# Kernel tuning notes

Measured on AMD Instinct MI355X. Metric: run time of the kernel, lower is better.

## Reference

```python
import math
import jax, jax.numpy as jnp
import numpy as np

FILTER_ORDER = 64
FILTER_EMB_DIM = 5
HIDDEN = 256
SHIFT = 0.05
FAST_DECAY_PCT = 0.3
SLOW_DECAY_PCT = 1.5
TARGET = 0.01


def setup_inputs() -> dict:
    key = jax.random.key(0)
    ks = jax.random.split(key, 8)
    B, C, L = 8, HIDDEN, 8192

    def lin_w(k, fan_out, fan_in):
        return jax.random.normal(k, (fan_out, fan_in), jnp.float32) / np.sqrt(fan_in).astype(np.float32)

    return {
        "x": jax.random.normal(ks[0], (B, C, L), jnp.float32),
        "W1": lin_w(ks[1], FILTER_ORDER, FILTER_EMB_DIM),
        "b1": jnp.zeros((FILTER_ORDER,), jnp.float32),
        "freq0": jnp.ones((1, FILTER_ORDER), jnp.float32),
        "W2": lin_w(ks[2], FILTER_ORDER, FILTER_ORDER),
        "b2": jnp.zeros((FILTER_ORDER,), jnp.float32),
        "freq1": jnp.ones((1, FILTER_ORDER), jnp.float32),
        "W3": lin_w(ks[3], FILTER_ORDER, FILTER_ORDER),
        "b3": jnp.zeros((FILTER_ORDER,), jnp.float32),
        "freq2": jnp.ones((1, FILTER_ORDER), jnp.float32),
        "Wout": lin_w(ks[4], HIDDEN, FILTER_ORDER),
        "D": jax.random.normal(ks[5], (HIDDEN,), jnp.float32),
        "L": L,
    }


def _pos_emb(L):
    # HyenaDnaPositionalEmbedding: z (1, L, emb_dim), t (1, L, 1)
    t = jnp.linspace(0.0, 1.0, L, dtype=jnp.float32)[None, :, None]
    t_rescaled = jnp.linspace(0.0, L - 1, L, dtype=jnp.float32)[None, :, None]
    w = 2.0 * math.pi * t_rescaled / L  # (1, L, 1)
    bands = (FILTER_EMB_DIM - 1) // 2
    f = jnp.linspace(1e-4, bands - 1, bands, dtype=jnp.float32)[None, None]  # (1, 1, bands)
    z = jnp.concatenate([t, jnp.cos(-f * w), jnp.sin(-f * w)], axis=-1)  # (1, L, emb_dim)
    return z, t


def _filter_kernel(W1, b1, freq0, W2, b2, freq1, W3, b3, freq2, Wout, L):
    z, t = _pos_emb(L)
    h = jnp.sin(freq0 * (jnp.einsum('ble,oe->blo', z, W1) + b1))
    h = jnp.sin(freq1 * (jnp.einsum('blo,po->blp', h, W2) + b2))
    h = jnp.sin(freq2 * (jnp.einsum('blo,po->blp', h, W3) + b3))
    h = jnp.einsum('blo,do->bld', h, Wout)  # (1, L, HIDDEN)
    # exponential modulation window
    max_decay = math.log(TARGET) / FAST_DECAY_PCT
    min_decay = math.log(TARGET) / SLOW_DECAY_PCT
    deltas = jnp.linspace(min_decay, max_decay, HIDDEN, dtype=jnp.float32)[None, None]
    decay = jnp.exp(-t * jnp.abs(deltas))  # (1, L, HIDDEN)
    h = h * (decay + SHIFT)
    return h[0].T  # (HIDDEN, L) channels-major kernel


def _fftconv(u, k, D):
    # y = conv(u, k) + u * D via FFT, zero-padded to 2L (linear convolution)
    L = u.shape[-1]
    fft_size = 2 * L
    k_f = jnp.fft.rfft(k.astype(jnp.float32), n=fft_size) / fft_size  # (C, fft_size//2+1)
    u_f = jnp.fft.rfft(u.astype(jnp.float32), n=fft_size)             # (B, C, fft_size//2+1)
    y = jnp.fft.irfft(u_f * k_f, n=fft_size, norm='forward')[..., :L]
    return (y + u * D[:, None]).astype(u.dtype)


def reference(x, W1, b1, freq0, W2, b2, freq1, W3, b3, freq2, Wout, D, L):
    k = _filter_kernel(W1, b1, freq0, W2, b2, freq1, W3, b3, freq2, Wout, L)
    return _fftconv(x, k, D)
```

## Files before the change

### kernel.cpp

```cpp
#include <hip/hip_runtime.h>

#define L_SEQ 8192
#define NTH 512
#define HID 256
#define PIDX(i) ((i) + ((i) >> 4))
#define LDS_SZ 8704

#define ANG16 3.83495196971410315e-4f
#define ANG8  7.66990393942820630e-4f
#define CS16 0.99999992646571789f
#define SN16 3.83495187571395563e-4f
#define CS8  0.99999970586287223f
#define SN8  7.66990318742704490e-4f
#define C707 0.70710678118654752f

__device__ __forceinline__ float2 cmul(float2 a, float2 b) {
  return make_float2(a.x*b.x - a.y*b.y, a.x*b.y + a.y*b.x);
}
__device__ __forceinline__ float2 cadd(float2 a, float2 b){ return make_float2(a.x+b.x, a.y+b.y); }
__device__ __forceinline__ float2 csub(float2 a, float2 b){ return make_float2(a.x-b.x, a.y-b.y); }

__device__ __forceinline__ void bf4_fwd(float2 a0, float2 a1, float2 a2, float2 a3,
                                        float2& o0, float2& o1, float2& o2, float2& o3) {
  float2 t0 = cadd(a0,a2), t1 = csub(a0,a2), t2 = cadd(a1,a3), t3 = csub(a1,a3);
  o0 = cadd(t0,t2);
  o2 = csub(t0,t2);
  o1 = make_float2(t1.x + t3.y, t1.y - t3.x);
  o3 = make_float2(t1.x - t3.y, t1.y + t3.x);
}
__device__ __forceinline__ void bf4_inv(float2 c0, float2 c1, float2 c2, float2 c3,
                                        float2& o0, float2& o1, float2& o2, float2& o3) {
  float2 u0 = cadd(c0,c2), u2 = csub(c0,c2), u1 = cadd(c1,c3);
  float2 v3 = make_float2(c3.y - c1.y, c1.x - c3.x);
  o0 = cadd(u0,u1); o2 = csub(u0,u1); o1 = cadd(u2,v3); o3 = csub(u2,v3);
}

__device__ __forceinline__ void fwd8(float2 P[8]) {
  float2 e0=cadd(P[0],P[4]), e1=cadd(P[1],P[5]), e2=cadd(P[2],P[6]), e3=cadd(P[3],P[7]);
  float2 o0=csub(P[0],P[4]), o1=csub(P[1],P[5]), o2=csub(P[2],P[6]), o3=csub(P[3],P[7]);
  o1 = make_float2((o1.x+o1.y)*C707, (o1.y-o1.x)*C707);
  o2 = make_float2(o2.y, -o2.x);
  o3 = make_float2((o3.y-o3.x)*C707, -(o3.x+o3.y)*C707);
  float2 q0,q1,q2,q3;
  bf4_fwd(e0,e1,e2,e3,q0,q1,q2,q3);
  P[0]=q0; P[2]=q1; P[4]=q2; P[6]=q3;
  bf4_fwd(o0,o1,o2,o3,q0,q1,q2,q3);
  P[1]=q0; P[3]=q1; P[5]=q2; P[7]=q3;
}
__device__ __forceinline__ void inv8(float2 P[8]) {
  float2 E0,E1,E2,E3,O0,O1,O2,O3;
  bf4_inv(P[0],P[2],P[4],P[6],E0,E1,E2,E3);
  bf4_inv(P[1],P[3],P[5],P[7],O0,O1,O2,O3);
  O1 = make_float2((O1.x-O1.y)*C707, (O1.x+O1.y)*C707);
  O2 = make_float2(-O2.y, O2.x);
  O3 = make_float2(-(O3.x+O3.y)*C707, (O3.x-O3.y)*C707);
  P[0]=cadd(E0,O0); P[4]=csub(E0,O0);
  P[1]=cadd(E1,O1); P[5]=csub(E1,O1);
  P[2]=cadd(E2,O2); P[6]=csub(E2,O2);
  P[3]=cadd(E3,O3); P[7]=csub(E3,O3);
}

template<int M>
__device__ __forceinline__ void fwd_stage8(float2* __restrict__ X, int t) {
  #pragma unroll
  for (int r = 0; r < 2; ++r) {
    int s = t + NTH*r;
    int i2 = s & (M-1);
    int g  = s / M;
    int base = g*8*M + i2;
    float2 P[8];
    #pragma unroll
    for (int j=0;j<8;++j) P[j] = X[PIDX(base + j*M)];
    fwd8(P);
    float sb, cb;
    __sincosf(-6.2831853071795864769f * (float)i2 / (float)(8*M), &sb, &cb);
    float2 w1 = make_float2(cb, sb);
    float2 w2 = cmul(w1,w1), w3 = cmul(w2,w1), w4 = cmul(w2,w2);
    float2 w5 = cmul(w4,w1), w6 = cmul(w4,w2), w7 = cmul(w4,w3);
    X[PIDX(base)]     = P[0];
    X[PIDX(base+M)]   = cmul(P[1],w1);
    X[PIDX(base+2*M)] = cmul(P[2],w2);
    X[PIDX(base+3*M)] = cmul(P[3],w3);
    X[PIDX(base+4*M)] = cmul(P[4],w4);
    X[PIDX(base+5*M)] = cmul(P[5],w5);
    X[PIDX(base+6*M)] = cmul(P[6],w6);
    X[PIDX(base+7*M)] = cmul(P[7],w7);
  }
}
template<int M>
__device__ __forceinline__ void inv_stage8(float2* __restrict__ X, int t) {
  #pragma unroll
  for (int r = 0; r < 2; ++r) {
    int s = t + NTH*r;
    int i2 = s & (M-1);
    int g  = s / M;
    int base = g*8*M + i2;
    float sb, cb;
    __sincosf(6.2831853071795864769f * (float)i2 / (float)(8*M), &sb, &cb);
    float2 w1 = make_float2(cb, sb);
    float2 w2 = cmul(w1,w1), w3 = cmul(w2,w1), w4 = cmul(w2,w2);
    float2 w5 = cmul(w4,w1), w6 = cmul(w4,w2), w7 = cmul(w4,w3);
    float2 P[8];
    P[0] = X[PIDX(base)];
    P[1] = cmul(X[PIDX(base+M)],  w1);
    P[2] = cmul(X[PIDX(base+2*M)],w2);
    P[3] = cmul(X[PIDX(base+3*M)],w3);
    P[4] = cmul(X[PIDX(base+4*M)],w4);
    P[5] = cmul(X[PIDX(base+5*M)],w5);
    P[6] = cmul(X[PIDX(base+6*M)],w6);
    P[7] = cmul(X[PIDX(base+7*M)],w7);
    inv8(P);
    #pragma unroll
    for (int j=0;j<8;++j) X[PIDX(base + j*M)] = P[j];
  }
}

__device__ __forceinline__ void fft_mid_fwd(float2* __restrict__ X, int t) {
  __syncthreads();
  fwd_stage8<512>(X,t); __syncthreads();
  fwd_stage8<64>(X,t);  __syncthreads();
  fwd_stage8<8>(X,t);   __syncthreads();
}
__device__ __forceinline__ void fft_mid_inv(float2* __restrict__ X, int t) {
  __syncthreads();
  inv_stage8<8>(X,t);   __syncthreads();
  inv_stage8<64>(X,t);  __syncthreads();
  inv_stage8<512>(X,t); __syncthreads();
}

__device__ __forceinline__ void middle_pointwise(float2* __restrict__ X,
                                                 const float2* __restrict__ K, int t) {
  #pragma unroll
  for (int r = 0; r < 2; ++r) {
    int base = 8*(t + NTH*r);
    float2 kreg[8];
    #pragma unroll
    for (int q=0;q<8;++q) kreg[q] = K[base+q];
    float2 P[8];
    #pragma unroll
    for (int q=0;q<8;++q) P[q] = X[PIDX(base+q)];
    fwd8(P);
    #pragma unroll
    for (int q=0;q<8;++q) P[q] = cmul(P[q], kreg[q]);
    inv8(P);
    #pragma unroll
    for (int q=0;q<8;++q) X[PIDX(base+q)] = P[q];
  }
}

__global__ __launch_bounds__(256) void mlp_kernel(
    const float* __restrict__ W1, const float* __restrict__ b1, const float* __restrict__ fq0,
    const float* __restrict__ W2, const float* __restrict__ b2, const float* __restrict__ fq1,
    const float* __restrict__ W3, const float* __restrict__ b3, const float* __restrict__ fq2,
    float* __restrict__ h3g) {
  __shared__ float hs[2][16][64];
  int tid = threadIdx.x;
  int lane = tid & 63, w = tid >> 6;
  int l0 = blockIdx.x * 16;

  float w1r[5];
  #pragma unroll
  for (int e = 0; e < 5; ++e) w1r[e] = W1[lane*5+e];
  float b1v = b1[lane], f0 = fq0[lane];
  #pragma unroll
  for (int r = 0; r < 4; ++r) {
    int l = l0 + w + 4*r;
    float t = (float)l * (1.0f / (float)(L_SEQ - 1));
    float ang = 6.2831853071795864769f * (float)l / (float)L_SEQ;
    float s0, c0, s1, c1;
    __sincosf(1e-4f * ang, &s0, &c0);
    __sincosf(ang, &s1, &c1);
    float acc = b1v + t*w1r[0] + c0*w1r[1] + c1*w1r[2] - s0*w1r[3] - s1*w1r[4];
    hs[0][w + 4*r][lane] = __sinf(f0 * acc);
  }
  __syncthreads();

  float wr[64];
  #pragma unroll
  for (int j = 0; j < 16; ++j) *(float4*)&wr[4*j] = *(const float4*)&W2[lane*64 + 4*j];
  float b2v = b2[lane], f1 = fq1[lane];
  #pragma unroll
  for (int r = 0; r < 4; ++r) {
    int ll = w + 4*r;
    float a0 = 0.f, a1 = 0.f, a2 = 0.f, a3 = 0.f;
    #pragma unroll
    for (int o = 0; o < 64; o += 4) {
      a0 += hs[0][ll][o+0] * wr[o+0];
      a1 += hs[0][ll][o+1] * wr[o+1];
      a2 += hs[0][ll][o+2] * wr[o+2];
      a3 += hs[0][ll][o+3] * wr[o+3];
    }
    hs[1][ll][lane] = __sinf(f1 * (b2v + ((a0+a1)+(a2+a3))));
  }
  __syncthreads();

  #pragma unroll
  for (int j = 0; j < 16; ++j) *(float4*)&wr[4*j] = *(const float4*)&W3[lane*64 + 4*j];
  float b3v = b3[lane], f2 = fq2[lane];
  #pragma unroll
  for (int r = 0; r < 4; ++r) {
    int ll = w + 4*r;
    float a0 = 0.f, a1 = 0.f, a2 = 0.f, a3 = 0.f;
    #pragma unroll
    for (int o = 0; o < 64; o += 4) {
      a0 += hs[1][ll][o+0] * wr[o+0];
      a1 += hs[1][ll][o+1] * wr[o+1];
      a2 += hs[1][ll][o+2] * wr[o+2];
      a3 += hs[1][ll][o+3] * wr[o+3];
    }
    h3g[(size_t)(l0 + ll) * 64 + lane] = __sinf(f2 * (b3v + ((a0+a1)+(a2+a3))));
  }
}

__global__ __launch_bounds__(256) void kwrite_kernel(const float* __restrict__ h3g,
                                                     const float* __restrict__ Wout,
                                                     const float* __restrict__ Dv,
                                                     float* __restrict__ kbuf) {
  __shared__ float tileh[256][65];
  int tid = threadIdx.x;
  int l0 = blockIdx.x * 256;
  int c0 = blockIdx.y * 32;
  {
    const float4* src = (const float4*)(h3g + (size_t)l0 * 64);
    #pragma unroll
    for (int q = 0; q < 16; ++q) {
      int idx = tid + 256*q;
      int row = idx >> 4, col4 = idx & 15;
      float4 v = src[idx];
      tileh[row][col4*4+0] = v.x;
      tileh[row][col4*4+1] = v.y;
      tileh[row][col4*4+2] = v.z;
      tileh[row][col4*4+3] = v.w;
    }
  }
  __syncthreads();
  float hr[64];
  #pragma unroll
  for (int o = 0; o < 64; ++o) hr[o] = tileh[tid][o];
  int l = l0 + tid;
  float t = (float)l * (1.0f / (float)(L_SEQ - 1));
  const float mind = -3.0701134573253945f;
  const float maxd = -15.350567286626972f;
  for (int jj = 0; jj < 32; ++jj) {
    int c = c0 + jj;
    float a0 = 0.f, a1 = 0.f, a2 = 0.f, a3 = 0.f;
    #pragma unroll
    for (int o = 0; o < 64; o += 4) {
      a0 += hr[o+0] * Wout[c*64+o+0];
      a1 += hr[o+1] * Wout[c*64+o+1];
      a2 += hr[o+2] * Wout[c*64+o+2];
      a3 += hr[o+3] * Wout[c*64+o+3];
    }
    float acc = (a0+a1)+(a2+a3);
    float delta = mind + (maxd - mind) * ((float)c * (1.0f/255.0f));
    float dec = __expf(-t * fabsf(delta)) + 0.05f;
    float v = acc * dec;
    if (l == 0) v += Dv[c];
    kbuf[(size_t)c * L_SEQ + l] = v;
  }
}

__global__ __launch_bounds__(NTH) void kf_kernel(const float* __restrict__ kbuf,
                                                 float2* __restrict__ Kf) {
  __shared__ float2 X[LDS_SZ];
  int pipe = blockIdx.x;
  int c = blockIdx.y;
  int t = threadIdx.x;
  const float* kr = kbuf + (size_t)c * L_SEQ;
  const float sc = 1.0f / 16384.0f;
  #pragma unroll
  for (int r = 0; r < 2; ++r) {
    int n0 = 4*t + 2048*r;
    float4 lo4 = *(const float4*)(kr + n0);
    float4 hi4 = *(const float4*)(kr + n0 + 4096);
    if (pipe == 0) {
      float sb, cb; __sincosf(-ANG8 * (float)n0, &sb, &cb);
      float2 w8 = make_float2(cb, sb);
      #pragma unroll
      for (int j = 0; j < 4; ++j) {
        if (j) w8 = cmul(w8, make_float2(CS8, -SN8));
        float klo = ((const float*)&lo4)[j];
        float khi = ((const float*)&hi4)[j];
        X[PIDX(n0+j)]      = make_float2(klo + khi, 0.f);
        float d = klo - khi;
        X[PIDX(n0+j+4096)] = make_float2(d * w8.x, d * w8.y);
      }
    } else {
      float sb, cb; __sincosf(-ANG16 * (float)n0, &sb, &cb);
      float2 w16 = make_float2(cb, sb);
      #pragma unroll
      for (int j = 0; j < 4; ++j) {
        if (j) w16 = cmul(w16, make_float2(CS16, -SN16));
        float klo = ((const float*)&lo4)[j];
        float khi = ((const float*)&hi4)[j];
        float2 vlo = make_float2(klo * w16.x, klo * w16.y);
        float2 vhi = make_float2(khi * w16.y, -khi * w16.x);
        float2 w8 = cmul(w16, w16);
        X[PIDX(n0+j)]      = cadd(vlo, vhi);
        X[PIDX(n0+j+4096)] = cmul(csub(vlo, vhi), w8);
      }
    }
  }
  fft_mid_fwd(X, t);
  #pragma unroll
  for (int r = 0; r < 2; ++r) {
    int base = 8*(t + NTH*r);
    float2 P[8];
    #pragma unroll
    for (int q=0;q<8;++q) P[q] = X[PIDX(base+q)];
    fwd8(P);
    float2* out = Kf + (size_t)c * 16384 + pipe*8192 + base;
    #pragma unroll
    for (int q=0;q<8;++q) out[q] = make_float2(P[q].x*sc, P[q].y*sc);
  }
}

__global__ __launch_bounds__(NTH) void conv_kernel(const float* __restrict__ x,
                                                   const float2* __restrict__ Kf,
                                                   float* __restrict__ y) {
  __shared__ float2 X[LDS_SZ];
  int c = blockIdx.x;
  int p = blockIdx.y;
  int t = threadIdx.x;
  const float* u0 = x + ((size_t)p       * HID + c) * L_SEQ;
  const float* u1 = x + ((size_t)(p + 4) * HID + c) * L_SEQ;
  const float2* KA = Kf + (size_t)c * 16384;
  const float2* KB = KA + 8192;
  float* y0 = y + ((size_t)p       * HID + c) * L_SEQ;
  float* y1 = y + ((size_t)(p + 4) * HID + c) * L_SEQ;

  #pragma unroll
  for (int r = 0; r < 2; ++r) {
    int n0 = 4*t + 2048*r;
    float4 a0 = *(const float4*)(u0 + n0);
    float4 a1 = *(const float4*)(u1 + n0);
    float4 b0 = *(const float4*)(u0 + n0 + 4096);
    float4 b1 = *(const float4*)(u1 + n0 + 4096);
    float sb, cb; __sincosf(-ANG16 * (float)n0, &sb, &cb);
    float2 w16 = make_float2(cb, sb);
    #pragma unroll
    for (int j = 0; j < 4; ++j) {
      if (j) w16 = cmul(w16, make_float2(CS16, -SN16));
      float2 vlo = cmul(make_float2(((const float*)&a0)[j], ((const float*)&a1)[j]), w16);
      float2 vhi = cmul(make_float2(((const float*)&b0)[j], ((const float*)&b1)[j]),
                        make_float2(w16.y, -w16.x));
      float2 w8 = cmul(w16, w16);
      X[PIDX(n0+j)]      = cadd(vlo, vhi);
      X[PIDX(n0+j+4096)] = cmul(csub(vlo, vhi), w8);
    }
  }
  fft_mid_fwd(X, t);
  middle_pointwise(X, KB, t);
  fft_mid_inv(X, t);
  float2 stash[16];
  #pragma unroll
  for (int r = 0; r < 2; ++r) {
    int n0 = 4*t + 2048*r;
    float sb, cb; __sincosf(ANG16 * (float)n0, &sb, &cb);
    float2 w16b = make_float2(cb, sb);
    #pragma unroll
    for (int j = 0; j < 4; ++j) {
      if (j) w16b = cmul(w16b, make_float2(CS16, SN16));
      float2 P = X[PIDX(n0+j)], Q = X[PIDX(n0+j+4096)];
      float2 w8b = cmul(w16b, w16b);
      float2 tt = cmul(Q, w8b);
      stash[r*4+j]     = cmul(cadd(P, tt), w16b);
      stash[8 + r*4+j] = cmul(csub(P, tt), make_float2(-w16b.y, w16b.x));
    }
  }
  __syncthreads();

  #pragma unroll
  for (int r = 0; r < 2; ++r) {
    int n0 = 4*t + 2048*r;
    float4 a0 = *(const float4*)(u0 + n0);
    float4 a1 = *(const float4*)(u1 + n0);
    float4 b0 = *(const float4*)(u0 + n0 + 4096);
    float4 b1 = *(const float4*)(u1 + n0 + 4096);
    float sb, cb; __sincosf(-ANG8 * (float)n0, &sb, &cb);
    float2 w8 = make_float2(cb, sb);
    #pragma unroll
    for (int j = 0; j < 4; ++j) {
      if (j) w8 = cmul(w8, make_float2(CS8, -SN8));
      float2 vlo = make_float2(((const float*)&a0)[j], ((const float*)&a1)[j]);
      float2 vhi = make_float2(((const float*)&b0)[j], ((const float*)&b1)[j]);
      X[PIDX(n0+j)]      = cadd(vlo, vhi);
      X[PIDX(n0+j+4096)] = cmul(csub(vlo, vhi), w8);
    }
  }
  fft_mid_fwd(X, t);
  middle_pointwise(X, KA, t);
  fft_mid_inv(X, t);
  #pragma unroll
  for (int r = 0; r < 2; ++r) {
    int n0 = 4*t + 2048*r;
    float sb, cb; __sincosf(ANG8 * (float)n0, &sb, &cb);
    float2 w8b = make_float2(cb, sb);
    float4 w00, w01, w10, w11;
    #pragma unroll
    for (int j = 0; j < 4; ++j) {
      if (j) w8b = cmul(w8b, make_float2(CS8, SN8));
      float2 P = X[PIDX(n0+j)], Q = X[PIDX(n0+j+4096)];
      float2 tt = cmul(Q, w8b);
      float2 lo = cadd(cadd(P, tt), stash[r*4+j]);
      float2 hi = cadd(csub(P, tt), stash[8 + r*4+j]);
      ((float*)&w00)[j] = lo.x; ((float*)&w01)[j] = lo.y;
      ((float*)&w10)[j] = hi.x; ((float*)&w11)[j] = hi.y;
    }
    *(float4*)(y0 + n0)        = w00;
    *(float4*)(y1 + n0)        = w01;
    *(float4*)(y0 + n0 + 4096) = w10;
    *(float4*)(y1 + n0 + 4096) = w11;
  }
}

extern "C" void kernel_launch(void* const* d_in, const int* in_sizes, int n_in,
                              void* d_out, int out_size, void* d_ws, size_t ws_size,
                              hipStream_t stream) {
  const float* x    = (const float*)d_in[0];
  const float* W1   = (const float*)d_in[1];
  const float* b1   = (const float*)d_in[2];
  const float* fq0  = (const float*)d_in[3];
  const float* W2   = (const float*)d_in[4];
  const float* b2   = (const float*)d_in[5];
  const float* fq1  = (const float*)d_in[6];
  const float* W3   = (const float*)d_in[7];
  const float* b3   = (const float*)d_in[8];
  const float* fq2  = (const float*)d_in[9];
  const float* Wout = (const float*)d_in[10];
  const float* Dv   = (const float*)d_in[11];

  float*  kbuf = (float*)d_ws;
  float2* Kf   = (float2*)((char*)d_ws + (size_t)HID * L_SEQ * sizeof(float));
  float*  h3g  = (float*)((char*)d_ws + 38ull*1024*1024);
  float*  y    = (float*)d_out;

  mlp_kernel   <<<dim3(512),   256, 0, stream>>>(W1,b1,fq0,W2,b2,fq1,W3,b3,fq2,h3g);
  kwrite_kernel<<<dim3(32, 8), 256, 0, stream>>>(h3g, Wout, Dv, kbuf);
  kf_kernel    <<<dim3(2, 256), NTH, 0, stream>>>(kbuf, Kf);
  conv_kernel  <<<dim3(256, 4), NTH, 0, stream>>>(x, Kf, y);
}
```

Before: 165.7 us.

## Vectorize radix-8 FFT stages with paired float4 LDS access and spill partial output to global

Changes LDS padding to two floats every 32 elements so adjacent complex pairs stay 16-byte aligned. The M=512 and M=64 stages now process two adjacent butterflies per thread using float4 LDS loads and stores, with the second twiddle derived by a constant rotation. The 16-element register stash that held the first half's result is removed: partial outputs are written to global y and re-read and accumulated after the second pass. This cuts register pressure and LDS instruction count, at the cost of extra global memory traffic.

```diff
diff --git a/kernel.cpp b/kernel.cpp
--- a/kernel.cpp
+++ b/kernel.cpp
@@ -3,7 +3,7 @@
 #define L_SEQ 8192
 #define NTH 512
 #define HID 256
-#define PIDX(i) ((i) + ((i) >> 4))
+#define PIDX(i) ((i) + (((i) >> 5) << 1))
 #define LDS_SZ 8704
 
 #define ANG16 3.83495196971410315e-4f
@@ -58,6 +58,71 @@
   P[1]=cadd(E1,O1); P[5]=csub(E1,O1);
   P[2]=cadd(E2,O2); P[6]=csub(E2,O2);
   P[3]=cadd(E3,O3); P[7]=csub(E3,O3);
+}
+
+template<int M> struct WS;
+template<> struct WS<512> { static constexpr float c = 0.99999882345170188f, s = 1.53398018628476561e-3f; };
+template<> struct WS<64>  { static constexpr float c = 0.99992470183914454f, s = 1.22715382857199261e-2f; };
+
+template<int M>
+__device__ __forceinline__ void fwd_stage8p(float2* __restrict__ X, int t) {
+  const int HM = M/2;
+  int g = t / HM;
+  int v = t - g*HM;
+  int i2 = 2*v;
+  int base = g*8*M + i2;
+  float2 P[8], Q[8];
+  #pragma unroll
+  for (int j=0;j<8;++j) {
+    float4 w = *(const float4*)&X[PIDX(base + j*M)];
+    P[j] = make_float2(w.x, w.y);
+    Q[j] = make_float2(w.z, w.w);
+  }
+  fwd8(P); fwd8(Q);
+  float sb, cb;
+  __sincosf(-6.2831853071795864769f * (float)i2 / (float)(8*M), &sb, &cb);
+  float2 wp1 = make_float2(cb, sb);
+  float2 wq1 = cmul(wp1, make_float2(WS<M>::c, -WS<M>::s));
+  *(float4*)&X[PIDX(base)] = make_float4(P[0].x, P[0].y, Q[0].x, Q[0].y);
+  float2 wp = wp1, wq = wq1;
+  #pragma unroll
+  for (int j=1;j<8;++j) {
+    float2 a = cmul(P[j], wp);
+    float2 b = cmul(Q[j], wq);
+    *(float4*)&X[PIDX(base + j*M)] = make_float4(a.x, a.y, b.x, b.y);
+    wp = cmul(wp, wp1);
+    wq = cmul(wq, wq1);
+  }
+}
+template<int M>
+__device__ __forceinline__ void inv_stage8p(float2* __restrict__ X, int t) {
+  const int HM = M/2;
+  int g = t / HM;
+  int v = t - g*HM;
+  int i2 = 2*v;
+  int base = g*8*M + i2;
+  float sb, cb;
+  __sincosf(6.2831853071795864769f * (float)i2 / (float)(8*M), &sb, &cb);
+  float2 wp1 = make_float2(cb, sb);
+  float2 wq1 = cmul(wp1, make_float2(WS<M>::c, WS<M>::s));
+  float2 P[8], Q[8];
+  {
+    float4 w = *(const float4*)&X[PIDX(base)];
+    P[0] = make_float2(w.x,w.y); Q[0] = make_float2(w.z,w.w);
+  }
+  float2 wp = wp1, wq = wq1;
+  #pragma unroll
+  for (int j=1;j<8;++j) {
+    float4 w = *(const float4*)&X[PIDX(base + j*M)];
+    P[j] = cmul(make_float2(w.x,w.y), wp);
+    Q[j] = cmul(make_float2(w.z,w.w), wq);
+    wp = cmul(wp, wp1);
+    wq = cmul(wq, wq1);
+  }
+  inv8(P); inv8(Q);
+  #pragma unroll
+  for (int j=0;j<8;++j)
+    *(float4*)&X[PIDX(base + j*M)] = make_float4(P[j].x,P[j].y,Q[j].x,Q[j].y);
 }
 
 template<int M>
@@ -117,15 +182,15 @@
 
 __device__ __forceinline__ void fft_mid_fwd(float2* __restrict__ X, int t) {
   __syncthreads();
-  fwd_stage8<512>(X,t); __syncthreads();
-  fwd_stage8<64>(X,t);  __syncthreads();
-  fwd_stage8<8>(X,t);   __syncthreads();
+  fwd_stage8p<512>(X,t); __syncthreads();
+  fwd_stage8p<64>(X,t);  __syncthreads();
+  fwd_stage8<8>(X,t);    __syncthreads();
 }
 __device__ __forceinline__ void fft_mid_inv(float2* __restrict__ X, int t) {
   __syncthreads();
-  inv_stage8<8>(X,t);   __syncthreads();
-  inv_stage8<64>(X,t);  __syncthreads();
-  inv_stage8<512>(X,t); __syncthreads();
+  inv_stage8<8>(X,t);    __syncthreads();
+  inv_stage8p<64>(X,t);  __syncthreads();
+  inv_stage8p<512>(X,t); __syncthreads();
 }
 
 __device__ __forceinline__ void middle_pointwise(float2* __restrict__ X,
@@ -352,21 +417,27 @@
   fft_mid_fwd(X, t);
   middle_pointwise(X, KB, t);
   fft_mid_inv(X, t);
-  float2 stash[16];
   #pragma unroll
   for (int r = 0; r < 2; ++r) {
     int n0 = 4*t + 2048*r;
     float sb, cb; __sincosf(ANG16 * (float)n0, &sb, &cb);
     float2 w16b = make_float2(cb, sb);
+    float4 w00, w01, w10, w11;
     #pragma unroll
     for (int j = 0; j < 4; ++j) {
       if (j) w16b = cmul(w16b, make_float2(CS16, SN16));
       float2 P = X[PIDX(n0+j)], Q = X[PIDX(n0+j+4096)];
       float2 w8b = cmul(w16b, w16b);
       float2 tt = cmul(Q, w8b);
-      stash[r*4+j]     = cmul(cadd(P, tt), w16b);
-      stash[8 + r*4+j] = cmul(csub(P, tt), make_float2(-w16b.y, w16b.x));
-    }
+      float2 lo = cmul(cadd(P, tt), w16b);
+      float2 hi = cmul(csub(P, tt), make_float2(-w16b.y, w16b.x));
+      ((float*)&w00)[j] = lo.x; ((float*)&w01)[j] = lo.y;
+      ((float*)&w10)[j] = hi.x; ((float*)&w11)[j] = hi.y;
+    }
+    *(float4*)(y0 + n0)        = w00;
+    *(float4*)(y1 + n0)        = w01;
+    *(float4*)(y0 + n0 + 4096) = w10;
+    *(float4*)(y1 + n0 + 4096) = w11;
   }
   __syncthreads();
 
@@ -394,6 +465,10 @@
   #pragma unroll
   for (int r = 0; r < 2; ++r) {
     int n0 = 4*t + 2048*r;
+    float4 p00 = *(const float4*)(y0 + n0);
+    float4 p01 = *(const float4*)(y1 + n0);
+    float4 p10 = *(const float4*)(y0 + n0 + 4096);
+    float4 p11 = *(const float4*)(y1 + n0 + 4096);
     float sb, cb; __sincosf(ANG8 * (float)n0, &sb, &cb);
     float2 w8b = make_float2(cb, sb);
     float4 w00, w01, w10, w11;
@@ -402,10 +477,12 @@
       if (j) w8b = cmul(w8b, make_float2(CS8, SN8));
       float2 P = X[PIDX(n0+j)], Q = X[PIDX(n0+j+4096)];
       float2 tt = cmul(Q, w8b);
-      float2 lo = cadd(cadd(P, tt), stash[r*4+j]);
-      float2 hi = cadd(csub(P, tt), stash[8 + r*4+j]);
-      ((float*)&w00)[j] = lo.x; ((float*)&w01)[j] = lo.y;
-      ((float*)&w10)[j] = hi.x; ((float*)&w11)[j] = hi.y;
+      float2 lo = cadd(P, tt);
+      float2 hi = csub(P, tt);
+      ((float*)&w00)[j] = lo.x + ((const float*)&p00)[j];
+      ((float*)&w01)[j] = lo.y + ((const float*)&p01)[j];
+      ((float*)&w10)[j] = hi.x + ((const float*)&p10)[j];
+      ((float*)&w11)[j] = hi.y + ((const float*)&p11)[j];
     }
     *(float4*)(y0 + n0)        = w00;
     *(float4*)(y1 + n0)        = w01;
```

Result: slower. 215.2 us (+29.9%).
